# Optimization experiments

Measured on AMD Instinct MI355X. Metric: run time of the kernel, lower is better.

## Reference

```python
import jax, jax.numpy as jnp
import numpy as np

N = 100000      # nodes
E = 640000      # edges
IN = 100        # in_channels
OUT = 128       # out_channels
H, D = 4, 32    # heads, per-head dim (OUT = H*D)
MSG, TOUT, ETD, NET = 16, 100, 8, 4
EDGE_COLS = MSG + TOUT + 2        # 118 raw edge_attr columns
EDIM = (MSG - 1) + ETD + TOUT + 2 # 125 processed edge feature dim
SCALE = 1.0 / np.sqrt(D)


def _lin(k, fi, fo):
    return (jax.random.normal(k, (fi, fo), jnp.float32) / np.sqrt(fi)).astype(jnp.float32)


def setup_inputs() -> dict:
    key = jax.random.key(0)
    ks = jax.random.split(key, 24)
    x = jax.random.normal(ks[0], (N, IN), jnp.float32)
    edge_index = jax.random.randint(ks[1], (2, E), 0, N, dtype=jnp.int32)
    ea = jax.random.normal(ks[2], (E, EDGE_COLS), jnp.float32)
    etype = jax.random.randint(ks[3], (E,), 0, NET).astype(jnp.float32)
    edge_attr = ea.at[:, 3].set(etype)
    emb = jax.random.normal(ks[4], (NET, ETD), jnp.float32)
    inp = {"x": x, "edge_index": edge_index, "edge_attr": edge_attr, "emb": emb}
    # conv1: in=IN, conv2: in=OUT; lin_edge has no bias (PyG default)
    for i, fi in ((1, IN), (2, OUT)):
        base = 5 + (i - 1) * 8
        inp[f"w{i}q"] = _lin(ks[base + 0], fi, OUT)
        inp[f"b{i}q"] = jnp.zeros((OUT,), jnp.float32)
        inp[f"w{i}k"] = _lin(ks[base + 1], fi, OUT)
        inp[f"b{i}k"] = jnp.zeros((OUT,), jnp.float32)
        inp[f"w{i}v"] = _lin(ks[base + 2], fi, OUT)
        inp[f"b{i}v"] = jnp.zeros((OUT,), jnp.float32)
        inp[f"w{i}e"] = _lin(ks[base + 3], EDIM, OUT)
        inp[f"w{i}s"] = _lin(ks[base + 4], fi, OUT)
        inp[f"b{i}s"] = jnp.zeros((OUT,), jnp.float32)
    return inp


def _seg_softmax(logits, seg, n):
    # logits: [E, H], softmax over edges sharing the same target node
    m = jax.ops.segment_max(logits, seg, num_segments=n)      # [N, H]
    ex = jnp.exp(logits - m[seg])
    s = jax.ops.segment_sum(ex, seg, num_segments=n)          # [N, H]
    return ex / (s[seg] + 1e-16)


def _tconv(x, src, dst, e, wq, bq, wk, bk, wv, bv, we, ws, bs):
    n = x.shape[0]
    q = (x @ wq + bq)[dst].reshape(-1, H, D)   # gather targets
    k = (x @ wk + bk)[src].reshape(-1, H, D)   # gather sources
    v = (x @ wv + bv)[src].reshape(-1, H, D)
    ee = (e @ we).reshape(-1, H, D)            # per-edge projection
    alpha = jnp.sum(q * (k + ee), axis=-1) * SCALE          # [E, H]
    a = _seg_softmax(alpha, dst, n)                          # scatter-softmax
    msg = (v + ee) * a[..., None]                            # [E, H, D]
    out = jax.ops.segment_sum(msg, dst, num_segments=n).reshape(n, H * D)
    return out + x @ ws + bs                                 # root/skip connection


def reference(x, edge_index, edge_attr, emb,
              w1q, b1q, w1k, b1k, w1v, b1v, w1e, w1s, b1s,
              w2q, b2q, w2k, b2k, w2v, b2v, w2e, w2s, b2s):
    src, dst = edge_index[0], edge_index[1]
    cont = edge_attr[:, :3]
    etype = edge_attr[:, 3].astype(jnp.int32)
    rest = edge_attr[:, 4:]
    e = jnp.concatenate([cont, rest, emb[etype]], axis=-1)   # [E, EDIM]
    h = jax.nn.relu(_tconv(x, src, dst, e, w1q, b1q, w1k, b1k, w1v, b1v, w1e, w1s, b1s))
    return _tconv(h, src, dst, e, w2q, b2q, w2k, b2k, w2v, b2v, w2e, w2s, b2s)
```

## Files before the change

### kernel.cpp

```cpp
#include <hip/hip_runtime.h>

#define NN 100000
#define NE 640000
#define OUTF 128
#define K1 100
#define KE 118
#define KPAD 128
#define ASTR 136
#define ATT_SCALE 0.17677669529663687f
#define NSCANB 391
#define ETILES 5

typedef __attribute__((ext_vector_type(8))) short short8;
typedef __attribute__((ext_vector_type(4))) float f32x4;

__device__ __forceinline__ unsigned short f2bf(float f) {
    unsigned u = __float_as_uint(f);
    u += 0x7FFFu + ((u >> 16) & 1u);
    return (unsigned short)(u >> 16);
}
__device__ __forceinline__ float bf2f(unsigned short h) {
    return __uint_as_float(((unsigned)h) << 16);
}

__global__ void prep_weights(
    const float* __restrict__ w1q, const float* __restrict__ w1k,
    const float* __restrict__ w1v, const float* __restrict__ w1s,
    const float* __restrict__ w2q, const float* __restrict__ w2k,
    const float* __restrict__ w2v, const float* __restrict__ w2s,
    const float* __restrict__ we1, const float* __restrict__ we2,
    const float* __restrict__ emb,
    const float* __restrict__ b1q, const float* __restrict__ b1k,
    const float* __restrict__ b1v, const float* __restrict__ b1s,
    const float* __restrict__ b2q, const float* __restrict__ b2k,
    const float* __restrict__ b2v, const float* __restrict__ b2s,
    unsigned short* __restrict__ WT1, unsigned short* __restrict__ WT2,
    unsigned short* __restrict__ WmT1, unsigned short* __restrict__ WmT2,
    float* __restrict__ bias1, float* __restrict__ bias2)
{
    int idx = blockIdx.x * blockDim.x + threadIdx.x;
    int stride = gridDim.x * blockDim.x;
    for (int i = idx; i < 512 * KPAD; i += stride) {
        int col = i >> 7, k = i & 127;
        int which = col >> 7, c = col & 127;
        const float* s1 = (which == 0) ? w1q : (which == 1) ? w1k : (which == 2) ? w1v : w1s;
        const float* s2 = (which == 0) ? w2q : (which == 1) ? w2k : (which == 2) ? w2v : w2s;
        float v1 = (k < K1) ? s1[k * OUTF + c] : 0.f;
        float v2 = s2[k * OUTF + c];
        WT1[i] = f2bf(v1); WT2[i] = f2bf(v2);
    }
    for (int i = idx; i < OUTF * KPAD; i += stride) {
        int col = i >> 7, k = i & 127;
        float v1 = 0.f, v2 = 0.f;
        if (k < 3)                 { v1 = we1[k * OUTF + col];       v2 = we2[k * OUTF + col]; }
        else if (k >= 4 && k < KE) { v1 = we1[(k - 1) * OUTF + col]; v2 = we2[(k - 1) * OUTF + col]; }
        else if (k >= KE && k < KE + 4) {
            int t = k - KE;
            #pragma unroll
            for (int r = 0; r < 8; r++) {
                float ev = emb[t * 8 + r];
                v1 += ev * we1[(117 + r) * OUTF + col];
                v2 += ev * we2[(117 + r) * OUTF + col];
            }
        }
        WmT1[i] = f2bf(v1); WmT2[i] = f2bf(v2);
    }
    for (int i = idx; i < 512; i += stride) {
        int which = i >> 7, c = i & 127;
        const float* sb1 = (which == 0) ? b1q : (which == 1) ? b1k : (which == 2) ? b1v : b1s;
        const float* sb2 = (which == 0) ? b2q : (which == 1) ? b2k : (which == 2) ? b2v : b2s;
        bias1[i] = sb1[c]; bias2[i] = sb2[c];
    }
}

__global__ void hist_kernel(const int* __restrict__ dstI, int* __restrict__ cnt) {
    int e = blockIdx.x * 256 + threadIdx.x;
    if (e < NE) atomicAdd(&cnt[dstI[e]], 1);
}
__global__ void scan1(const int* __restrict__ cnt, int* __restrict__ S1, int* __restrict__ bsum) {
    __shared__ int sd[256];
    int t = blockIdx.x * 256 + threadIdx.x;
    sd[threadIdx.x] = (t < NN) ? cnt[t] : 0;
    __syncthreads();
    for (int off = 1; off < 256; off <<= 1) {
        int x = (threadIdx.x >= off) ? sd[threadIdx.x - off] : 0;
        __syncthreads();
        sd[threadIdx.x] += x;
        __syncthreads();
    }
    if (t < NN) S1[t] = sd[threadIdx.x];
    if (threadIdx.x == 255) bsum[blockIdx.x] = sd[255];
}
__global__ void scan2(const int* __restrict__ bsum, int* __restrict__ boff) {
    __shared__ int sd[512];
    int t = threadIdx.x;
    sd[t] = (t < NSCANB) ? bsum[t] : 0;
    __syncthreads();
    for (int off = 1; off < 512; off <<= 1) {
        int x = (t >= off) ? sd[t - off] : 0;
        __syncthreads();
        sd[t] += x;
        __syncthreads();
    }
    if (t < NSCANB) boff[t] = (t == 0) ? 0 : sd[t - 1];
}
__global__ void scan3(const int* __restrict__ S1, const int* __restrict__ boff,
                      const int* __restrict__ cnt,
                      int* __restrict__ row_start, int* __restrict__ cursor) {
    int t = blockIdx.x * 256 + threadIdx.x;
    if (t < NN) {
        int incl = S1[t] + boff[t >> 8];
        row_start[t + 1] = incl;
        cursor[t] = incl - cnt[t];
        if (t == 0) row_start[0] = 0;
    }
}
__global__ void scatter_csr(const int* __restrict__ srcI, const int* __restrict__ dstI,
                            int* __restrict__ cursor, int2* __restrict__ csr_pair) {
    int e = blockIdx.x * 256 + threadIdx.x;
    if (e < NE) {
        int j = atomicAdd(&cursor[dstI[e]], 1);
        csr_pair[j] = make_int2(srcI[e], e);
    }
}

__global__ __launch_bounds__(256) void node_mfma(
    const float* __restrict__ X, int ldx, int Kdim, int relu, int n,
    const unsigned short* __restrict__ WT, const float* __restrict__ bias,
    float* __restrict__ Qp, unsigned short* __restrict__ KVp, float* __restrict__ Hp)
{
    __shared__ unsigned short Alds[128][ASTR];
    int tid = threadIdx.x;
    int rowbase = (blockIdx.x >> 2) * 128;
    int nb = blockIdx.x & 3;

    for (int idx = tid; idx < 128 * 68; idx += 256) {
        int r = idx / 68, kv = idx % 68;
        int k = kv * 2;
        float2 v = make_float2(0.f, 0.f);
        int gr = rowbase + r;
        if (gr < n && k < Kdim) v = *(const float2*)(X + (size_t)gr * ldx + k);
        if (relu) { v.x = fmaxf(v.x, 0.f); v.y = fmaxf(v.y, 0.f); }
        unsigned pv = (unsigned)f2bf(v.x) | ((unsigned)f2bf(v.y) << 16);
        *(unsigned*)&Alds[r][k] = pv;
    }
    __syncthreads();

    int lane = tid & 63, wid = tid >> 6;
    int wm = wid >> 1, wn = wid & 1;
    int l15 = lane & 15, l4 = lane >> 4;

    f32x4 acc[4][4];
    #pragma unroll
    for (int mf = 0; mf < 4; mf++)
        #pragma unroll
        for (int nf = 0; nf < 4; nf++)
            acc[mf][nf] = (f32x4){0.f, 0.f, 0.f, 0.f};

    const unsigned short* wbase = WT + (size_t)(nb * 128 + wn * 64 + l15) * KPAD + l4 * 8;
    #pragma unroll
    for (int ks = 0; ks < 4; ks++) {
        short8 af[4], bfr[4];
        #pragma unroll
        for (int mf = 0; mf < 4; mf++)
            af[mf] = *(const short8*)&Alds[wm * 64 + mf * 16 + l15][ks * 32 + l4 * 8];
        #pragma unroll
        for (int nf = 0; nf < 4; nf++)
            bfr[nf] = *(const short8*)(wbase + (size_t)nf * 16 * KPAD + ks * 32);
        #pragma unroll
        for (int mf = 0; mf < 4; mf++)
            #pragma unroll
            for (int nf = 0; nf < 4; nf++)
                acc[mf][nf] = __builtin_amdgcn_mfma_f32_16x16x32_bf16(af[mf], bfr[nf], acc[mf][nf], 0, 0, 0);
    }
    __syncthreads();

    if (nb == 1 || nb == 2) {
        #pragma unroll
        for (int nf = 0; nf < 4; nf++) {
            int col = wn * 64 + nf * 16 + l15;
            float bv = bias[nb * 128 + col];
            #pragma unroll
            for (int mf = 0; mf < 4; mf++)
                #pragma unroll
                for (int rr = 0; rr < 4; rr++)
                    Alds[wm * 64 + mf * 16 + l4 * 4 + rr][col] = f2bf(acc[mf][nf][rr] + bv);
        }
        __syncthreads();
        int off = (nb == 1) ? 0 : 128;
        #pragma unroll
        for (int it = 0; it < 8; it++) {
            int idx = it * 256 + tid;
            int row = idx >> 4, c8 = (idx & 15) * 8;
            if (rowbase + row < n) {
                uint4 v = *(const uint4*)&Alds[row][c8];
                *(uint4*)(KVp + (size_t)(rowbase + row) * 256 + off + c8) = v;
            }
        }
    } else {
        float* Yp = (nb == 0) ? Qp : Hp;
        float scale = (nb == 0) ? ATT_SCALE : 1.f;
        float (*Sf)[68] = (float (*)[68])Alds;
        #pragma unroll
        for (int h = 0; h < 2; h++) {
            if (wn == h) {
                #pragma unroll
                for (int nf = 0; nf < 4; nf++) {
                    int col = wn * 64 + nf * 16 + l15;
                    float bv = bias[nb * 128 + col];
                    #pragma unroll
                    for (int mf = 0; mf < 4; mf++)
                        #pragma unroll
                        for (int rr = 0; rr < 4; rr++)
                            Sf[wm * 64 + mf * 16 + l4 * 4 + rr][nf * 16 + l15] =
                                (acc[mf][nf][rr] + bv) * scale;
                }
            }
            __syncthreads();
            #pragma unroll
            for (int it = 0; it < 8; it++) {
                int idx = it * 256 + tid;
                int row = idx >> 4, c4 = (idx & 15) * 4;
                if (rowbase + row < n) {
                    float4 v = *(const float4*)&Sf[row][c4];
                    *(float4*)(Yp + (size_t)(rowbase + row) * OUTF + h * 64 + c4) = v;
                }
            }
            if (h == 0) __syncthreads();
        }
    }
}

__global__ __launch_bounds__(256) void edge_mfma_fused(
    const float* __restrict__ EA,
    const unsigned short* __restrict__ WmT1, const unsigned short* __restrict__ WmT2,
    unsigned short* __restrict__ EE1, unsigned short* __restrict__ EE2)
{
    __shared__ unsigned short Tlds[64][ASTR];
    int tid = threadIdx.x;
    int lane = tid & 63, w = tid >> 6;
    int l15 = lane & 15, l4 = lane >> 4;
    int rbase = w * 16;
    int tile0 = blockIdx.x * ETILES;

    auto load_tile = [&](int tile, short8* af) {
        const float* rp = EA + (size_t)(tile * 64 + rbase + l15) * KE;
        float etf = rp[3];
        #pragma unroll
        for (int ks = 0; ks < 4; ks++) {
            int cbase = ks * 32 + l4 * 8;
            float2 t0 = make_float2(0.f, 0.f), t1 = t0, t2 = t0, t3 = t0;
            if (cbase + 2 <= KE) t0 = *(const float2*)(rp + cbase);
            if (cbase + 4 <= KE) t1 = *(const float2*)(rp + cbase + 2);
            if (cbase + 6 <= KE) t2 = *(const float2*)(rp + cbase + 4);
            if (cbase + 8 <= KE) t3 = *(const float2*)(rp + cbase + 6);
            float fv[8] = {t0.x, t0.y, t1.x, t1.y, t2.x, t2.y, t3.x, t3.y};
            #pragma unroll
            for (int j = 0; j < 8; j++) {
                int col = cbase + j;
                float v = (col == 3) ? 0.f : fv[j];
                af[ks][j] = f2bf(v);
            }
        }
        int oh = KE + (int)etf;
        #pragma unroll
        for (int j = 0; j < 8; j++) {
            int col = 96 + l4 * 8 + j;
            if (col == oh) af[3][j] = 0x3F80;
        }
    };
    auto do_layer = [&](const unsigned short* __restrict__ WmT, unsigned short* __restrict__ EEc,
                        int e0, const short8* af) {
        f32x4 acc[8];
        #pragma unroll
        for (int nf = 0; nf < 8; nf++) acc[nf] = (f32x4){0.f, 0.f, 0.f, 0.f};

        #pragma unroll
        for (int ks = 0; ks < 4; ks++) {
            short8 bfr[8];
            #pragma unroll
            for (int nf = 0; nf < 8; nf++)
                bfr[nf] = *(const short8*)(WmT + (size_t)(nf * 16 + l15) * KPAD + ks * 32 + l4 * 8);
            #pragma unroll
            for (int nf = 0; nf < 8; nf++)
                acc[nf] = __builtin_amdgcn_mfma_f32_16x16x32_bf16(af[ks], bfr[nf], acc[nf], 0, 0, 0);
        }
        #pragma unroll
        for (int nf = 0; nf < 8; nf++)
            #pragma unroll
            for (int rr = 0; rr < 4; rr++)
                Tlds[rbase + l4 * 4 + rr][nf * 16 + l15] = f2bf(acc[nf][rr]);
        #pragma unroll
        for (int it = 0; it < 4; it++) {
            int t2 = it * 64 + lane;
            int rid = t2 >> 4, c8 = (t2 & 15) * 8;
            uint4 v = *(const uint4*)&Tlds[rbase + rid][c8];
            *(uint4*)(EEc + ((size_t)(e0 + rbase + rid)) * 128 + c8) = v;
        }
    };

    short8 afA[4];
    load_tile(tile0, afA);

    #pragma unroll
    for (int t = 0; t < ETILES; t++) {
        int e0 = (tile0 + t) * 64;
        do_layer(WmT1, EE1, e0, afA);
        short8 afB[4];
        if (t + 1 < ETILES) load_tile(tile0 + t + 1, afB);
        do_layer(WmT2, EE2, e0, afA);
        if (t + 1 < ETILES) {
            afA[0] = afB[0]; afA[1] = afB[1]; afA[2] = afB[2]; afA[3] = afB[3];
        }
    }
}

__global__ __launch_bounds__(256) void attn_node(
    const float* __restrict__ Qp, const unsigned short* __restrict__ KVp,
    const unsigned short* __restrict__ EEc,
    const int* __restrict__ row_start, const int2* __restrict__ csr_pair,
    const float* __restrict__ Hskip, float* __restrict__ Out)
{
    int lane = threadIdx.x & 63;
    int gw = (int)((blockIdx.x * (size_t)blockDim.x + threadIdx.x) >> 6);
    int nW = (gridDim.x * blockDim.x) >> 6;
    int c2 = lane * 2;

    for (int d = gw; d < NN; d += nW) {
        int rs = row_start[d], re = row_start[d + 1];
        float2 q = *(const float2*)(Qp + (size_t)d * OUTF + c2);
        float m = -3.4e38f, s = 0.f, a0 = 0.f, a1 = 0.f;

        int j0 = (rs < re) ? rs : 0;
        int jlast = (rs < re) ? re - 1 : 0;
        int j1 = (j0 + 1 <= jlast) ? j0 + 1 : jlast;
        int j2 = (j0 + 2 <= jlast) ? j0 + 2 : jlast;
        int2 prA = csr_pair[j0];
        int2 prB = csr_pair[j1];
        int2 prC = csr_pair[j2];
        unsigned kA = *(const unsigned*)(KVp + (size_t)prA.x * 256 + c2);
        unsigned vA = *(const unsigned*)(KVp + (size_t)prA.x * 256 + 128 + c2);
        unsigned eA = *(const unsigned*)(EEc + (size_t)prA.y * 128 + c2);
        unsigned kB = *(const unsigned*)(KVp + (size_t)prB.x * 256 + c2);
        unsigned vB = *(const unsigned*)(KVp + (size_t)prB.x * 256 + 128 + c2);
        unsigned eB = *(const unsigned*)(EEc + (size_t)prB.y * 128 + c2);

        for (int j = rs; j < re; j++) {
            unsigned kC = *(const unsigned*)(KVp + (size_t)prC.x * 256 + c2);
            unsigned vC = *(const unsigned*)(KVp + (size_t)prC.x * 256 + 128 + c2);
            unsigned eC = *(const unsigned*)(EEc + (size_t)prC.y * 128 + c2);
            int j3 = (j + 3 <= jlast) ? j + 3 : jlast;
            int2 prD = csr_pair[j3];

            float e0 = bf2f((unsigned short)(eA & 0xFFFFu));
            float e1 = bf2f((unsigned short)(eA >> 16));
            float k0 = bf2f((unsigned short)(kA & 0xFFFFu));
            float k1 = bf2f((unsigned short)(kA >> 16));
            float v0 = bf2f((unsigned short)(vA & 0xFFFFu));
            float v1 = bf2f((unsigned short)(vA >> 16));

            float t = q.x * (k0 + e0) + q.y * (k1 + e1);
            t += __shfl_xor(t, 1); t += __shfl_xor(t, 2);
            t += __shfl_xor(t, 4); t += __shfl_xor(t, 8);
            float alpha = t;
            float mn = fmaxf(m, alpha);
            float r = __expf(m - mn);
            float p = __expf(alpha - mn);
            s = s * r + p;
            a0 = a0 * r + p * (v0 + e0);
            a1 = a1 * r + p * (v1 + e1);
            m = mn;
            kA = kB; vA = vB; eA = eB;
            kB = kC; vB = vC; eB = eC;
            prC = prD;
        }
        float inv = 1.f / (s + 1e-16f);
        float2 h = *(const float2*)(Hskip + (size_t)d * OUTF + c2);
        float2 o;
        o.x = a0 * inv + h.x;
        o.y = a1 * inv + h.y;
        *(float2*)(Out + (size_t)d * OUTF + c2) = o;
    }
}

extern "C" void kernel_launch(void* const* d_in, const int* in_sizes, int n_in,
                              void* d_out, int out_size, void* d_ws, size_t ws_size,
                              hipStream_t stream) {
    const float* x    = (const float*)d_in[0];
    const int*   ei   = (const int*)d_in[1];
    const float* ea   = (const float*)d_in[2];
    const float* emb  = (const float*)d_in[3];
    const float* w1q  = (const float*)d_in[4];  const float* b1q = (const float*)d_in[5];
    const float* w1k  = (const float*)d_in[6];  const float* b1k = (const float*)d_in[7];
    const float* w1v  = (const float*)d_in[8];  const float* b1v = (const float*)d_in[9];
    const float* w1e  = (const float*)d_in[10];
    const float* w1s  = (const float*)d_in[11]; const float* b1s = (const float*)d_in[12];
    const float* w2q  = (const float*)d_in[13]; const float* b2q = (const float*)d_in[14];
    const float* w2k  = (const float*)d_in[15]; const float* b2k = (const float*)d_in[16];
    const float* w2v  = (const float*)d_in[17]; const float* b2v = (const float*)d_in[18];
    const float* w2e  = (const float*)d_in[19];
    const float* w2s  = (const float*)d_in[20]; const float* b2s = (const float*)d_in[21];

    const int* srcI = ei;
    const int* dstI = ei + NE;

    float* Q = (float*)d_ws;
    unsigned short* KV = (unsigned short*)(Q + (size_t)NN * OUTF);
    float* H = (float*)(KV + (size_t)NN * 256);
    unsigned short* EE1 = (unsigned short*)(H + (size_t)NN * OUTF);
    unsigned short* EE2 = EE1 + (size_t)NE * 128;
    int2* csr_pair = (int2*)(EE2 + (size_t)NE * 128);
    int* row_start = (int*)(csr_pair + NE);
    int* cursor    = row_start + NN + 1;
    int* cnt       = cursor + NN;
    int* S1        = cnt + NN;
    int* bsum      = S1 + NN;
    int* boff      = bsum + NSCANB;
    unsigned short* WT1  = (unsigned short*)(boff + NSCANB + 1);
    unsigned short* WT2  = WT1 + 512 * KPAD;
    unsigned short* WmT1 = WT2 + 512 * KPAD;
    unsigned short* WmT2 = WmT1 + OUTF * KPAD;
    float* bias1 = (float*)(WmT2 + OUTF * KPAD);
    float* bias2 = bias1 + 512;

    prep_weights<<<128, 256, 0, stream>>>(w1q, w1k, w1v, w1s, w2q, w2k, w2v, w2s,
                                          w1e, w2e, emb,
                                          b1q, b1k, b1v, b1s, b2q, b2k, b2v, b2s,
                                          WT1, WT2, WmT1, WmT2, bias1, bias2);
    hipMemsetAsync(cnt, 0, (size_t)NN * sizeof(int), stream);
    hist_kernel<<<NE / 256, 256, 0, stream>>>(dstI, cnt);
    scan1<<<NSCANB, 256, 0, stream>>>(cnt, S1, bsum);
    scan2<<<1, 512, 0, stream>>>(bsum, boff);
    scan3<<<NSCANB, 256, 0, stream>>>(S1, boff, cnt, row_start, cursor);
    scatter_csr<<<NE / 256, 256, 0, stream>>>(srcI, dstI, cursor, csr_pair);

    int ngrid = ((NN + 127) / 128) * 4;
    int egrid = NE / (64 * ETILES);

    node_mfma<<<ngrid, 256, 0, stream>>>(x, K1, K1, 0, NN, WT1, bias1, Q, KV, H);
    edge_mfma_fused<<<egrid, 256, 0, stream>>>(ea, WmT1, WmT2, EE1, EE2);
    attn_node<<<4096, 256, 0, stream>>>(Q, KV, EE1, row_start, csr_pair, H, H);

    node_mfma<<<ngrid, 256, 0, stream>>>(H, OUTF, OUTF, 1, NN, WT2, bias2, Q, KV, (float*)d_out);
    attn_node<<<4096, 256, 0, stream>>>(Q, KV, EE2, row_start, csr_pair, (float*)d_out, (float*)d_out);
}
```

Before: 977.4 us.

## Fuse layer-1 edge projection, node GEMM and CSR scatter into one launch

Merges the CSR scatter, the layer-1 node projection GEMM and the fused edge-attribute projection into a single kernel that routes work by block index. The independent workloads can then run concurrently, filling the GPU and removing launch gaps and tail idle between kernels. In exchange, every block reserves the larger 128-row LDS buffer, which may reduce occupancy for the edge and scatter portions.

```diff
diff --git a/kernel.cpp b/kernel.cpp
--- a/kernel.cpp
+++ b/kernel.cpp
@@ -10,6 +10,9 @@
 #define ATT_SCALE 0.17677669529663687f
 #define NSCANB 391
 #define ETILES 5
+#define EGRID 2000
+#define NGRID4 3128
+#define SGRID 2500
 
 typedef __attribute__((ext_vector_type(8))) short short8;
 typedef __attribute__((ext_vector_type(4))) float f32x4;
@@ -115,24 +118,16 @@
         if (t == 0) row_start[0] = 0;
     }
 }
-__global__ void scatter_csr(const int* __restrict__ srcI, const int* __restrict__ dstI,
-                            int* __restrict__ cursor, int2* __restrict__ csr_pair) {
-    int e = blockIdx.x * 256 + threadIdx.x;
-    if (e < NE) {
-        int j = atomicAdd(&cursor[dstI[e]], 1);
-        csr_pair[j] = make_int2(srcI[e], e);
-    }
-}
-
-__global__ __launch_bounds__(256) void node_mfma(
+
+__device__ __forceinline__ void node_body(
+    int nbid, unsigned short (*Alds)[ASTR],
     const float* __restrict__ X, int ldx, int Kdim, int relu, int n,
     const unsigned short* __restrict__ WT, const float* __restrict__ bias,
     float* __restrict__ Qp, unsigned short* __restrict__ KVp, float* __restrict__ Hp)
 {
-    __shared__ unsigned short Alds[128][ASTR];
     int tid = threadIdx.x;
-    int rowbase = (blockIdx.x >> 2) * 128;
-    int nb = blockIdx.x & 3;
+    int rowbase = (nbid >> 2) * 128;
+    int nb = nbid & 3;
 
     for (int idx = tid; idx < 128 * 68; idx += 256) {
         int r = idx / 68, kv = idx % 68;
@@ -231,17 +226,17 @@
     }
 }
 
-__global__ __launch_bounds__(256) void edge_mfma_fused(
+__device__ __forceinline__ void edge_body(
+    int ebid, unsigned short (*Tlds)[ASTR],
     const float* __restrict__ EA,
     const unsigned short* __restrict__ WmT1, const unsigned short* __restrict__ WmT2,
     unsigned short* __restrict__ EE1, unsigned short* __restrict__ EE2)
 {
-    __shared__ unsigned short Tlds[64][ASTR];
     int tid = threadIdx.x;
     int lane = tid & 63, w = tid >> 6;
     int l15 = lane & 15, l4 = lane >> 4;
     int rbase = w * 16;
-    int tile0 = blockIdx.x * ETILES;
+    int tile0 = ebid * ETILES;
 
     auto load_tile = [&](int tile, short8* af) {
         const float* rp = EA + (size_t)(tile * 64 + rbase + l15) * KE;
@@ -313,6 +308,40 @@
             afA[0] = afB[0]; afA[1] = afB[1]; afA[2] = afB[2]; afA[3] = afB[3];
         }
     }
+}
+
+__global__ __launch_bounds__(256) void mega_l1(
+    const float* __restrict__ EA,
+    const unsigned short* __restrict__ WmT1, const unsigned short* __restrict__ WmT2,
+    unsigned short* __restrict__ EE1, unsigned short* __restrict__ EE2,
+    const float* __restrict__ X,
+    const unsigned short* __restrict__ WT, const float* __restrict__ bias,
+    float* __restrict__ Qp, unsigned short* __restrict__ KVp, float* __restrict__ Hp,
+    const int* __restrict__ srcI, const int* __restrict__ dstI,
+    int* __restrict__ cursor, int2* __restrict__ csr_pair)
+{
+    __shared__ unsigned short Alds[128][ASTR];
+    int bid = blockIdx.x;
+    if (bid < EGRID) {
+        edge_body(bid, Alds, EA, WmT1, WmT2, EE1, EE2);
+    } else if (bid < EGRID + NGRID4) {
+        node_body(bid - EGRID, Alds, X, K1, K1, 0, NN, WT, bias, Qp, KVp, Hp);
+    } else {
+        int e = (bid - EGRID - NGRID4) * 256 + threadIdx.x;
+        if (e < NE) {
+            int j = atomicAdd(&cursor[dstI[e]], 1);
+            csr_pair[j] = make_int2(srcI[e], e);
+        }
+    }
+}
+
+__global__ __launch_bounds__(256) void node_mfma(
+    const float* __restrict__ X, int ldx, int Kdim, int relu, int n,
+    const unsigned short* __restrict__ WT, const float* __restrict__ bias,
+    float* __restrict__ Qp, unsigned short* __restrict__ KVp, float* __restrict__ Hp)
+{
+    __shared__ unsigned short Alds[128][ASTR];
+    node_body(blockIdx.x, Alds, X, ldx, Kdim, relu, n, WT, bias, Qp, KVp, Hp);
 }
 
 __global__ __launch_bounds__(256) void attn_node(
@@ -432,15 +461,14 @@
     scan1<<<NSCANB, 256, 0, stream>>>(cnt, S1, bsum);
     scan2<<<1, 512, 0, stream>>>(bsum, boff);
     scan3<<<NSCANB, 256, 0, stream>>>(S1, boff, cnt, row_start, cursor);
-    scatter_csr<<<NE / 256, 256, 0, stream>>>(srcI, dstI, cursor, csr_pair);
-
-    int ngrid = ((NN + 127) / 128) * 4;
-    int egrid = NE / (64 * ETILES);
-
-    node_mfma<<<ngrid, 256, 0, stream>>>(x, K1, K1, 0, NN, WT1, bias1, Q, KV, H);
-    edge_mfma_fused<<<egrid, 256, 0, stream>>>(ea, WmT1, WmT2, EE1, EE2);
+
+    mega_l1<<<EGRID + NGRID4 + SGRID, 256, 0, stream>>>(
+        ea, WmT1, WmT2, EE1, EE2,
+        x, WT1, bias1, Q, KV, H,
+        srcI, dstI, cursor, csr_pair);
+
     attn_node<<<4096, 256, 0, stream>>>(Q, KV, EE1, row_start, csr_pair, H, H);
 
-    node_mfma<<<ngrid, 256, 0, stream>>>(H, OUTF, OUTF, 1, NN, WT2, bias2, Q, KV, (float*)d_out);
+    node_mfma<<<NGRID4, 256, 0, stream>>>(H, OUTF, OUTF, 1, NN, WT2, bias2, Q, KV, (float*)d_out);
     attn_node<<<4096, 256, 0, stream>>>(Q, KV, EE2, row_start, csr_pair, (float*)d_out, (float*)d_out);
 }
```

After: 967.4 us, median of 2. About the same (-1.0%).
